# Performance work log

Hardware: AMD Instinct MI355X
Metric: run time of the kernel (lower is better)

Reference implementation:

```python
import jax, jax.numpy as jnp
import numpy as np

N, T, D = 128, 2048, 88

def setup_inputs() -> dict:
    key = jax.random.key(0)
    k1, k2 = jax.random.split(key)
    output = jax.random.normal(k1, (N, T, D), dtype=jnp.float32)
    # binary piano-roll style target (sparse note activations)
    target = (jax.random.uniform(k2, (N, T, D)) < 0.1).astype(jnp.float32)
    mask = jnp.ones((N, T), dtype=jnp.int32)  # left-aligned valid mask
    return {"output": output, "target": target, "mask": mask}

def reference(output, target, mask):
    # prediction = (sigmoid(output) > 0.5) -> non-differentiable 0/1 floats
    pred = (jax.nn.sigmoid(output) > 0.5).astype(output.dtype)
    # tru_pos summed over both feature and time dims -> [N]
    tru_pos = jnp.sum(pred * target, axis=(1, 2))
    # per-timestep false pos / false neg -> [N, T]
    false_pos = jnp.sum(pred * (1.0 - target), axis=2)
    false_neg = jnp.sum((1.0 - pred) * target, axis=2)
    # T_i = number of valid timesteps per sequence (loop runs over t < T_i)
    T_i = jnp.sum(mask, axis=1)  # [N] int
    valid = (jnp.arange(false_pos.shape[1])[None, :] < T_i[:, None]).astype(output.dtype)
    ratio = tru_pos[:, None] / (tru_pos[:, None] + false_pos + false_neg)  # [N, T]
    acc = jnp.sum(ratio * valid, axis=1) / T_i.astype(output.dtype)  # [N]
    return jnp.sum(acc)
```

## Files before the change

kernel.cpp:

```cpp
#include <hip/hip_runtime.h>
#include <stdint.h>

#define NN 128
#define TT 2048
#define DD 88
#define ROWS 32
#define TILES 4
#define TILES_TOTAL (NN * TT / ROWS)
#define K1_BLOCKS (TILES_TOTAL / TILES)
#define F4_TILE (ROWS * DD / 4)
#define PARTS_PER_N (TT / (ROWS * TILES))

typedef float f4 __attribute__((ext_vector_type(4)));
typedef const __attribute__((address_space(1))) uint32_t guint;
typedef __attribute__((address_space(3))) uint32_t luint;

__global__ __launch_bounds__(256) void acc_rowstats_kernel(
    const float* __restrict__ outp, const float* __restrict__ tgt,
    float* __restrict__ fpfn, float* __restrict__ tp_part) {
  __shared__ f4 lds_o[F4_TILE];
  __shared__ f4 lds_g[F4_TILE];
  __shared__ float s_tp[4];

  const int tid = threadIdx.x;
  const int lane = tid & 63;
  const int wave = tid >> 6;
  const int blk = blockIdx.x;
  const int r = tid >> 3;
  const int s = tid & 7;

  float tp = 0.f;
  for (int t4 = 0; t4 < TILES; ++t4) {
    const int tile = blk * TILES + t4;
    const size_t tile_f = (size_t)tile * (ROWS * DD);

    for (int j = wave; j < 22; j += 4) {
      const int is_g = (j >= 11) ? 1 : 0;
      const int idx = j - is_g * 11;
      const float* src = (is_g ? tgt : outp) + tile_f + idx * 256;
      float* dst = (is_g ? (float*)lds_g : (float*)lds_o) + idx * 256;
      __builtin_amdgcn_global_load_lds((guint*)src + lane * 4, (luint*)dst,
                                       16, 0, 0);
    }
    __syncthreads();

    float x = 0.f;
#pragma unroll
    for (int j0 = 0; j0 < 3; ++j0) {
      const int j = s + j0 * 8;
      if (j < 22) {
        const f4 o = lds_o[r * 22 + j];
        const f4 g = lds_g[r * 22 + j];
        {
          const float pf = (o.x > 0.f) ? 1.f : 0.f;
          x += fabsf(pf - g.x);
          tp = fmaf(pf, g.x, tp);
        }
        {
          const float pf = (o.y > 0.f) ? 1.f : 0.f;
          x += fabsf(pf - g.y);
          tp = fmaf(pf, g.y, tp);
        }
        {
          const float pf = (o.z > 0.f) ? 1.f : 0.f;
          x += fabsf(pf - g.z);
          tp = fmaf(pf, g.z, tp);
        }
        {
          const float pf = (o.w > 0.f) ? 1.f : 0.f;
          x += fabsf(pf - g.w);
          tp = fmaf(pf, g.w, tp);
        }
      }
    }
    x += __shfl_down(x, 4, 64);
    x += __shfl_down(x, 2, 64);
    x += __shfl_down(x, 1, 64);
    if (s == 0) fpfn[(size_t)tile * ROWS + r] = x;
    __syncthreads();
  }

  for (int off = 32; off > 0; off >>= 1) tp += __shfl_down(tp, off, 64);
  if (lane == 0) s_tp[wave] = tp;
  __syncthreads();
  if (tid == 0) tp_part[blk] = s_tp[0] + s_tp[1] + s_tp[2] + s_tp[3];
}

__global__ __launch_bounds__(256) void acc_finalize_kernel(
    const int* __restrict__ mask, const float* __restrict__ fpfn,
    const float* __restrict__ tp_part, float* __restrict__ out) {
  const int n = blockIdx.x;
  const int tid = threadIdx.x;
  __shared__ float sa[256], sb[256];

  const int4* m4 = (const int4*)(mask + (size_t)n * TT);
  int ti = 0;
#pragma unroll
  for (int it = 0; it < 2; ++it) {
    const int4 v = m4[it * 256 + tid];
    ti += v.x + v.y + v.z + v.w;
  }
  const float tpv = (tid < PARTS_PER_N) ? tp_part[n * PARTS_PER_N + tid] : 0.f;

  sa[tid] = (float)ti;
  sb[tid] = tpv;
  __syncthreads();
  for (int s = 128; s > 0; s >>= 1) {
    if (tid < s) { sa[tid] += sa[tid + s]; sb[tid] += sb[tid + s]; }
    __syncthreads();
  }
  const float fTi = sa[0];
  const float tp = sb[0];
  const int Ti = (int)fTi;
  __syncthreads();

  const float* __restrict__ fr = fpfn + (size_t)n * TT;
  float a = 0.f;
  for (int t = tid; t < Ti; t += 256) a += tp / (tp + fr[t]);
  sa[tid] = a;
  __syncthreads();
  for (int s = 128; s > 0; s >>= 1) {
    if (tid < s) sa[tid] += sa[tid + s];
    __syncthreads();
  }
  if (tid == 0) atomicAdd(out, sa[0] / fTi);
}

extern "C" void kernel_launch(void* const* d_in, const int* in_sizes, int n_in,
                              void* d_out, int out_size, void* d_ws, size_t ws_size,
                              hipStream_t stream) {
  const float* output = (const float*)d_in[0];
  const float* target = (const float*)d_in[1];
  const int* mask = (const int*)d_in[2];
  float* out = (float*)d_out;

  float* tp_part = (float*)d_ws;
  float* fpfn = tp_part + K1_BLOCKS;

  hipMemsetAsync(d_out, 0, sizeof(float) * out_size, stream);
  acc_rowstats_kernel<<<K1_BLOCKS, 256, 0, stream>>>(output, target, fpfn, tp_part);
  acc_finalize_kernel<<<NN, 256, 0, stream>>>(mask, fpfn, tp_part, out);
}
```

Baseline: 210.0 us.

## Fuse row-stats and finalize into one kernel using atomic tickets

Merges the two kernels into a single launch. The last block per sequence, found with an atomic ticket counter, computes that sequence's accuracy, and a second ticket picks the block that sums all sequences into the output. Each block now handles one tile instead of four, giving four times as many blocks. This removes a kernel launch and the gap between kernels, at the cost of atomics, relaxed-ordering memory visibility risk, and per-block tail work.

```diff
diff --git a/kernel.cpp b/kernel.cpp
--- a/kernel.cpp
+++ b/kernel.cpp
@@ -5,93 +5,109 @@
 #define TT 2048
 #define DD 88
 #define ROWS 32
-#define TILES 4
-#define TILES_TOTAL (NN * TT / ROWS)
-#define K1_BLOCKS (TILES_TOTAL / TILES)
 #define F4_TILE (ROWS * DD / 4)
-#define PARTS_PER_N (TT / (ROWS * TILES))
+#define K1_BLOCKS (NN * TT / ROWS)
+#define BLKS_PER_N (TT / ROWS)
 
 typedef float f4 __attribute__((ext_vector_type(4)));
 typedef const __attribute__((address_space(1))) uint32_t guint;
 typedef __attribute__((address_space(3))) uint32_t luint;
 
-__global__ __launch_bounds__(256) void acc_rowstats_kernel(
+#define TP_OFF 0
+#define TICKET_OFF 128
+#define TICKET2_OFF 256
+#define ACC_OFF 260
+#define FPFN_OFF 512
+
+__global__ __launch_bounds__(256) void acc_fused_kernel(
     const float* __restrict__ outp, const float* __restrict__ tgt,
-    float* __restrict__ fpfn, float* __restrict__ tp_part) {
+    const int* __restrict__ mask, float* __restrict__ ws,
+    float* __restrict__ resp) {
   __shared__ f4 lds_o[F4_TILE];
   __shared__ f4 lds_g[F4_TILE];
   __shared__ float s_tp[4];
+  __shared__ float sred[256];
+  __shared__ unsigned int s_old, s_old2;
+  __shared__ float s_tpn;
+
+  float* tp_total = ws + TP_OFF;
+  unsigned int* ticket = (unsigned int*)(ws + TICKET_OFF);
+  unsigned int* ticket2 = (unsigned int*)(ws + TICKET2_OFF);
+  float* acc = ws + ACC_OFF;
+  float* fpfn = ws + FPFN_OFF;
 
   const int tid = threadIdx.x;
   const int lane = tid & 63;
   const int wave = tid >> 6;
   const int blk = blockIdx.x;
+  const int n = blk >> 6;
+  const size_t tile_f = (size_t)blk * (ROWS * DD);
+
+  for (int j = wave; j < 22; j += 4) {
+    const int is_g = (j >= 11) ? 1 : 0;
+    const int idx = j - is_g * 11;
+    const float* src = (is_g ? tgt : outp) + tile_f + idx * 256;
+    float* dst = (is_g ? (float*)lds_g : (float*)lds_o) + idx * 256;
+    __builtin_amdgcn_global_load_lds((guint*)src + lane * 4, (luint*)dst,
+                                     16, 0, 0);
+  }
+  __syncthreads();
+
   const int r = tid >> 3;
   const int s = tid & 7;
-
   float tp = 0.f;
-  for (int t4 = 0; t4 < TILES; ++t4) {
-    const int tile = blk * TILES + t4;
-    const size_t tile_f = (size_t)tile * (ROWS * DD);
-
-    for (int j = wave; j < 22; j += 4) {
-      const int is_g = (j >= 11) ? 1 : 0;
-      const int idx = j - is_g * 11;
-      const float* src = (is_g ? tgt : outp) + tile_f + idx * 256;
-      float* dst = (is_g ? (float*)lds_g : (float*)lds_o) + idx * 256;
-      __builtin_amdgcn_global_load_lds((guint*)src + lane * 4, (luint*)dst,
-                                       16, 0, 0);
-    }
-    __syncthreads();
-
-    float x = 0.f;
+  float x = 0.f;
 #pragma unroll
-    for (int j0 = 0; j0 < 3; ++j0) {
-      const int j = s + j0 * 8;
-      if (j < 22) {
-        const f4 o = lds_o[r * 22 + j];
-        const f4 g = lds_g[r * 22 + j];
-        {
-          const float pf = (o.x > 0.f) ? 1.f : 0.f;
-          x += fabsf(pf - g.x);
-          tp = fmaf(pf, g.x, tp);
-        }
-        {
-          const float pf = (o.y > 0.f) ? 1.f : 0.f;
-          x += fabsf(pf - g.y);
-          tp = fmaf(pf, g.y, tp);
-        }
-        {
-          const float pf = (o.z > 0.f) ? 1.f : 0.f;
-          x += fabsf(pf - g.z);
-          tp = fmaf(pf, g.z, tp);
-        }
-        {
-          const float pf = (o.w > 0.f) ? 1.f : 0.f;
-          x += fabsf(pf - g.w);
-          tp = fmaf(pf, g.w, tp);
-        }
+  for (int j0 = 0; j0 < 3; ++j0) {
+    const int j = s + j0 * 8;
+    if (j < 22) {
+      const f4 o = lds_o[r * 22 + j];
+      const f4 g = lds_g[r * 22 + j];
+      {
+        const float pf = (o.x > 0.f) ? 1.f : 0.f;
+        x += fabsf(pf - g.x);
+        tp = fmaf(pf, g.x, tp);
+      }
+      {
+        const float pf = (o.y > 0.f) ? 1.f : 0.f;
+        x += fabsf(pf - g.y);
+        tp = fmaf(pf, g.y, tp);
+      }
+      {
+        const float pf = (o.z > 0.f) ? 1.f : 0.f;
+        x += fabsf(pf - g.z);
+        tp = fmaf(pf, g.z, tp);
+      }
+      {
+        const float pf = (o.w > 0.f) ? 1.f : 0.f;
+        x += fabsf(pf - g.w);
+        tp = fmaf(pf, g.w, tp);
       }
     }
-    x += __shfl_down(x, 4, 64);
-    x += __shfl_down(x, 2, 64);
-    x += __shfl_down(x, 1, 64);
-    if (s == 0) fpfn[(size_t)tile * ROWS + r] = x;
-    __syncthreads();
   }
+  x += __shfl_down(x, 4, 64);
+  x += __shfl_down(x, 2, 64);
+  x += __shfl_down(x, 1, 64);
+  if (s == 0)
+    __hip_atomic_store(&fpfn[(size_t)blk * ROWS + r], x, __ATOMIC_RELAXED,
+                       __HIP_MEMORY_SCOPE_AGENT);
 
   for (int off = 32; off > 0; off >>= 1) tp += __shfl_down(tp, off, 64);
   if (lane == 0) s_tp[wave] = tp;
+  __builtin_amdgcn_s_waitcnt(0);
   __syncthreads();
-  if (tid == 0) tp_part[blk] = s_tp[0] + s_tp[1] + s_tp[2] + s_tp[3];
-}
 
-__global__ __launch_bounds__(256) void acc_finalize_kernel(
-    const int* __restrict__ mask, const float* __restrict__ fpfn,
-    const float* __restrict__ tp_part, float* __restrict__ out) {
-  const int n = blockIdx.x;
-  const int tid = threadIdx.x;
-  __shared__ float sa[256], sb[256];
+  if (tid == 0) {
+    const float tpb = s_tp[0] + s_tp[1] + s_tp[2] + s_tp[3];
+    __hip_atomic_fetch_add(&tp_total[n], tpb, __ATOMIC_RELAXED,
+                           __HIP_MEMORY_SCOPE_AGENT);
+    __builtin_amdgcn_s_waitcnt(0);
+    s_old = __hip_atomic_fetch_add(&ticket[n], 1u, __ATOMIC_RELAXED,
+                                   __HIP_MEMORY_SCOPE_AGENT);
+  }
+  __syncthreads();
+  if (s_old != (unsigned)(BLKS_PER_N - 1)) return;
+
 
   const int4* m4 = (const int4*)(mask + (size_t)n * TT);
   int ti = 0;
@@ -100,30 +116,53 @@
     const int4 v = m4[it * 256 + tid];
     ti += v.x + v.y + v.z + v.w;
   }
-  const float tpv = (tid < PARTS_PER_N) ? tp_part[n * PARTS_PER_N + tid] : 0.f;
-
-  sa[tid] = (float)ti;
-  sb[tid] = tpv;
+  sred[tid] = (float)ti;
+  if (tid == 0)
+    s_tpn = __hip_atomic_load(&tp_total[n], __ATOMIC_RELAXED,
+                              __HIP_MEMORY_SCOPE_AGENT);
   __syncthreads();
-  for (int s = 128; s > 0; s >>= 1) {
-    if (tid < s) { sa[tid] += sa[tid + s]; sb[tid] += sb[tid + s]; }
+  for (int st = 128; st > 0; st >>= 1) {
+    if (tid < st) sred[tid] += sred[tid + st];
     __syncthreads();
   }
-  const float fTi = sa[0];
-  const float tp = sb[0];
+  const float fTi = sred[0];
   const int Ti = (int)fTi;
+  const float tpn = s_tpn;
   __syncthreads();
 
-  const float* __restrict__ fr = fpfn + (size_t)n * TT;
   float a = 0.f;
-  for (int t = tid; t < Ti; t += 256) a += tp / (tp + fr[t]);
-  sa[tid] = a;
+  const float* fr = fpfn + (size_t)n * TT;
+  for (int t = tid; t < Ti; t += 256) {
+    const float fv =
+        __hip_atomic_load(&fr[t], __ATOMIC_RELAXED, __HIP_MEMORY_SCOPE_AGENT);
+    a += tpn / (tpn + fv);
+  }
+  sred[tid] = a;
   __syncthreads();
-  for (int s = 128; s > 0; s >>= 1) {
-    if (tid < s) sa[tid] += sa[tid + s];
+  for (int st = 128; st > 0; st >>= 1) {
+    if (tid < st) sred[tid] += sred[tid + st];
     __syncthreads();
   }
-  if (tid == 0) atomicAdd(out, sa[0] / fTi);
+  if (tid == 0) {
+    __hip_atomic_store(&acc[n], sred[0] / fTi, __ATOMIC_RELAXED,
+                       __HIP_MEMORY_SCOPE_AGENT);
+    __builtin_amdgcn_s_waitcnt(0);
+    s_old2 = __hip_atomic_fetch_add(ticket2, 1u, __ATOMIC_RELAXED,
+                                    __HIP_MEMORY_SCOPE_AGENT);
+  }
+  __syncthreads();
+  if (s_old2 != (unsigned)(NN - 1)) return;
+
+  sred[tid] = (tid < NN)
+                  ? __hip_atomic_load(&acc[tid], __ATOMIC_RELAXED,
+                                      __HIP_MEMORY_SCOPE_AGENT)
+                  : 0.f;
+  __syncthreads();
+  for (int st = 128; st > 0; st >>= 1) {
+    if (tid < st) sred[tid] += sred[tid + st];
+    __syncthreads();
+  }
+  if (tid == 0) resp[0] = sred[0];
 }
 
 extern "C" void kernel_launch(void* const* d_in, const int* in_sizes, int n_in,
@@ -133,11 +172,8 @@
   const float* target = (const float*)d_in[1];
   const int* mask = (const int*)d_in[2];
   float* out = (float*)d_out;
+  float* ws = (float*)d_ws;
 
-  float* tp_part = (float*)d_ws;
-  float* fpfn = tp_part + K1_BLOCKS;
-
-  hipMemsetAsync(d_out, 0, sizeof(float) * out_size, stream);
-  acc_rowstats_kernel<<<K1_BLOCKS, 256, 0, stream>>>(output, target, fpfn, tp_part);
-  acc_finalize_kernel<<<NN, 256, 0, stream>>>(mask, fpfn, tp_part, out);
+  hipMemsetAsync(d_ws, 0, 512 * sizeof(float), stream);
+  acc_fused_kernel<<<K1_BLOCKS, 256, 0, stream>>>(output, target, mask, ws, out);
 }
```

New measurement: 226.9 us. 1.08x slower.
